# Kernel optimization log

Hardware: AMD Instinct MI355X
Metric: run time of the kernel (lower is better)

Reference implementation:

```python
import jax, jax.numpy as jnp
import numpy as np

NUM_HEADS = 8

def _proj(x, w, b):
    # 1x1x1 Conv3d == pointwise linear over channel dim
    return jnp.einsum('bcxyz,oc->boxyz', x, w) + b[None, :, None, None, None]


def setup_inputs() -> dict:
    key = jax.random.key(0)
    ks = jax.random.split(key, 9)
    B, C, X, Y, Z = 2, 256, 48, 48, 48
    s = 0.05
    return {
        'x':  jax.random.normal(ks[0], (B, C, X, Y, Z), dtype=jnp.float32),
        'wq': jax.random.normal(ks[1], (C, C), dtype=jnp.float32) * s,
        'bq': jax.random.normal(ks[2], (C,), dtype=jnp.float32) * s,
        'wk': jax.random.normal(ks[3], (C, C), dtype=jnp.float32) * s,
        'bk': jax.random.normal(ks[4], (C,), dtype=jnp.float32) * s,
        'wv': jax.random.normal(ks[5], (C, C), dtype=jnp.float32) * s,
        'bv': jax.random.normal(ks[6], (C,), dtype=jnp.float32) * s,
        'wo': jax.random.normal(ks[7], (C, C), dtype=jnp.float32) * s,
        'bo': jax.random.normal(ks[8], (C,), dtype=jnp.float32) * s,
    }


def reference(x, wq, bq, wk, bk, wv, bv, wo, bo):
    B, C, X, Y, Z = x.shape
    H = NUM_HEADS
    P = C // H  # per-head channels
    q = _proj(x, wq, bq).reshape(B, H, P, X, Y, Z)
    k = _proj(x, wk, bk).reshape(B, H, P, X, Y, Z)
    v = _proj(x, wv, bv).reshape(B, H, P, X, Y, Z)
    # torch einsum 'bnxyzc,bmxyzc->bnmxy' contracts z and per-head channel c
    scores = jnp.einsum('bncxyz,bmcxyz->bnmxy', q, k) / jnp.sqrt(jnp.float32(P))
    # torch F.softmax(dim=-1) on [b,n,m,x,y] -> softmax over y axis (faithful)
    attn = jax.nn.softmax(scores, axis=-1)
    # torch 'bnmxy,bmxyzc->bnxyzc', then permute/reshape back to [B,C,X,Y,Z]
    out = jnp.einsum('bnmxy,bmcxyz->bncxyz', attn, v).reshape(B, C, X, Y, Z)
    return _proj(out, wo, bo)
```

## Files before the change

kernel.cpp:

```cpp
#include <hip/hip_runtime.h>
#include <hip/hip_bf16.h>
#include <stdint.h>


#define S_TOT 110592
#define NBX   2304

typedef unsigned short u16;
typedef __attribute__((ext_vector_type(8))) short bf16x8;
typedef __attribute__((ext_vector_type(4))) float f32x4;

__device__ __forceinline__ u16 f2b(float f){
  union { float f; uint32_t u; } v; v.f = f;
  uint32_t u = v.u;
  return (u16)((u + 0x7fffu + ((u >> 16) & 1u)) >> 16);
}
__device__ __forceinline__ float b2f(u16 h){
  union { float f; uint32_t u; } v; v.u = ((uint32_t)h) << 16; return v.f;
}
__device__ __forceinline__ f32x4 mfma16(bf16x8 a, bf16x8 b, f32x4 c){
  return __builtin_amdgcn_mfma_f32_16x16x32_bf16(a, b, c, 0, 0, 0);
}

__global__ __launch_bounds__(256) void k_prep(
    const float* __restrict__ wq, const float* __restrict__ wk,
    const float* __restrict__ wv, const float* __restrict__ wo,
    u16* __restrict__ img)
{
  int idx = blockIdx.x * 256 + threadIdx.x;
  if (idx < 131072){
    int ck = idx >> 14, rem = idx & 16383;
    int r = rem >> 5, i = rem & 31;
    int c = ck * 32 + i;
    float v = (r < 256) ? wq[r * 256 + c] : wk[(r - 256) * 256 + c];
    img[idx] = f2b(v);
  } else if (idx < 196608){
    int l = idx - 131072;
    int ck = l >> 13, rem = l & 8191;
    int r = rem >> 5, i = rem & 31;
    img[idx] = f2b(wv[r * 256 + ck * 32 + i]);
  } else if (idx < 262144){
    int l = idx - 196608;
    int ck = l >> 13, rem = l & 8191;
    int r = rem >> 5, i = rem & 31;
    img[idx] = f2b(wo[r * 256 + ck * 32 + i]);
  }
}

#define K1_LDS 57344
__global__ __launch_bounds__(1024, 4) void k_qk_scores(
    const float* __restrict__ x, const u16* __restrict__ wimg,
    const float* __restrict__ bq, const float* __restrict__ bk,
    float* __restrict__ scores)
{
  extern __shared__ char lds[];
  u16* xT  = (u16*)lds;
  u16* qkz = (u16*)lds;
  float* ps0 = (float*)(lds + 49152);
  float* ps1 = (float*)(lds + 53248);

  const int tid  = threadIdx.x;
  const int wave = tid >> 6, lane = tid & 63;
  const int l15 = lane & 15, l4 = lane >> 4;
  const int bx = blockIdx.x, b = blockIdx.y;
  const int s0 = bx * 96;
  const float* xb = x + (size_t)b * 256 * S_TOT;

  #pragma unroll
  for (int it = 0; it < 3; it++){
    int e = it * 1024 + tid;
    int z = e % 96, c16 = e / 96;
    const float* px = xb + (size_t)(c16 * 8) * S_TOT + s0 + z;
    union { uint4 q; u16 h[8]; } u;
    #pragma unroll
    for (int i = 0; i < 8; i++) u.h[i] = f2b(px[(size_t)i * S_TOT]);
    *(uint4*)((char*)xT + z * 512 + ((c16 ^ (z & 7)) << 4)) = u.q;
  }
  __syncthreads();

  const int proj = wave >> 3;
  const int rb = (wave & 7) * 32;
  const float* bias = proj ? bk : bq;

  f32x4 acc[2][6];
  #pragma unroll
  for (int fr = 0; fr < 2; fr++){
    f32x4 iv;
    #pragma unroll
    for (int j = 0; j < 4; j++) iv[j] = bias[rb + fr * 16 + l4 * 4 + j];
    #pragma unroll
    for (int fc = 0; fc < 6; fc++) acc[fr][fc] = iv;
  }
  #pragma unroll
  for (int ck = 0; ck < 8; ck++){
    bf16x8 af[2], bfr[6];
    #pragma unroll
    for (int fr = 0; fr < 2; fr++){
      int row = wave * 32 + fr * 16 + l15;
      af[fr] = *(const bf16x8*)(wimg + ck * 16384 + row * 32 + l4 * 8);
    }
    #pragma unroll
    for (int fc = 0; fc < 6; fc++){
      int z = fc * 16 + l15;
      bfr[fc] = *(const bf16x8*)((char*)xT + z * 512 + (((ck * 4 + l4) ^ (l15 & 7)) << 4));
    }
    #pragma unroll
    for (int fr = 0; fr < 2; fr++)
      #pragma unroll
      for (int fc = 0; fc < 6; fc++)
        acc[fr][fc] = mfma16(af[fr], bfr[fc], acc[fr][fc]);
  }
  __syncthreads();

  const int och = proj * 256 + rb + l4 * 4;
  const int ca = l15 * 32 + l4 * 8;
  const int cb = 256 + (l15 & 7) * 32 + l4 * 8;

  #pragma unroll
  for (int fr = 0; fr < 2; fr++){
    int oc = och + fr * 16;
    #pragma unroll
    for (int fc = 0; fc < 3; fc++){
      int zl = fc * 16 + l15;
      ushort4 u;
      u.x = f2b(acc[fr][fc][0]); u.y = f2b(acc[fr][fc][1]);
      u.z = f2b(acc[fr][fc][2]); u.w = f2b(acc[fr][fc][3]);
      *(ushort4*)((char*)qkz + zl * 1024 + ((((oc >> 3) ^ zl) & 63) << 4)
                  + (oc & 7) * 2) = u;
    }
  }
  __syncthreads();
  {
    f32x4 sc = {0.f, 0.f, 0.f, 0.f};
    #pragma unroll
    for (int zi = 0; zi < 3; zi++){
      int zl = wave * 3 + zi;
      bf16x8 aq  = *(const bf16x8*)((char*)qkz + zl * 1024 + ((((ca >> 3) ^ zl) & 63) << 4));
      bf16x8 bk8 = *(const bf16x8*)((char*)qkz + zl * 1024 + ((((cb >> 3) ^ zl) & 63) << 4));
      sc = mfma16(aq, bk8, sc);
    }
    if (l4 < 2 && l15 < 8){
      #pragma unroll
      for (int j = 0; j < 4; j++)
        ps0[wave * 64 + (l4 * 4 + j) * 8 + l15] = sc[j];
    }
  }
  __syncthreads();

  if (tid < 64){
    float s = 0.f;
    #pragma unroll
    for (int w = 0; w < 16; w++) s += ps0[w * 64 + tid];
    scores[(size_t)(b * 64 + tid) * NBX + bx * 2] = s * 0.17677669529663687f;
  }
  #pragma unroll
  for (int fr = 0; fr < 2; fr++){
    int oc = och + fr * 16;
    #pragma unroll
    for (int fc = 3; fc < 6; fc++){
      int zl = (fc - 3) * 16 + l15;
      ushort4 u;
      u.x = f2b(acc[fr][fc][0]); u.y = f2b(acc[fr][fc][1]);
      u.z = f2b(acc[fr][fc][2]); u.w = f2b(acc[fr][fc][3]);
      *(ushort4*)((char*)qkz + zl * 1024 + ((((oc >> 3) ^ zl) & 63) << 4)
                  + (oc & 7) * 2) = u;
    }
  }
  __syncthreads();
  {
    f32x4 sc = {0.f, 0.f, 0.f, 0.f};
    #pragma unroll
    for (int zi = 0; zi < 3; zi++){
      int zl = wave * 3 + zi;
      bf16x8 aq  = *(const bf16x8*)((char*)qkz + zl * 1024 + ((((ca >> 3) ^ zl) & 63) << 4));
      bf16x8 bk8 = *(const bf16x8*)((char*)qkz + zl * 1024 + ((((cb >> 3) ^ zl) & 63) << 4));
      sc = mfma16(aq, bk8, sc);
    }
    if (l4 < 2 && l15 < 8){
      #pragma unroll
      for (int j = 0; j < 4; j++)
        ps1[wave * 64 + (l4 * 4 + j) * 8 + l15] = sc[j];
    }
  }
  __syncthreads();
  if (tid < 64){
    float s = 0.f;
    #pragma unroll
    for (int w = 0; w < 16; w++) s += ps1[w * 64 + tid];
    scores[(size_t)(b * 64 + tid) * NBX + bx * 2 + 1] = s * 0.17677669529663687f;
  }
}

__global__ __launch_bounds__(256) void k_softmax(
    const float* __restrict__ scores, float* __restrict__ attn)
{
  int row  = blockIdx.x * 4 + (threadIdx.x >> 6);
  int lane = threadIdx.x & 63;
  const float* src = scores + (size_t)row * 48;
  float v = (lane < 48) ? src[lane] : -1e30f;
  float m = v;
  #pragma unroll
  for (int off = 32; off; off >>= 1) m = fmaxf(m, __shfl_xor(m, off));
  float e = (lane < 48) ? __expf(v - m) : 0.f;
  float s = e;
  #pragma unroll
  for (int off = 32; off; off >>= 1) s += __shfl_xor(s, off);
  if (lane < 48) attn[(size_t)row * 48 + lane] = e / s;
}

#define K3_LDS 49664
__global__ __launch_bounds__(512, 4) void k_out(
    const float* __restrict__ x, const u16* __restrict__ wvimg,
    const u16* __restrict__ woimg, const float* __restrict__ bv,
    const float* __restrict__ bo, const float* __restrict__ attn,
    float* __restrict__ out)
{
  extern __shared__ char lds[];
  u16* xT = (u16*)lds;
  u16* vl = (u16*)lds;
  u16* oT = (u16*)lds;
  float* atl = (float*)(lds + 49152);

  const int tid  = threadIdx.x;
  const int wave = tid >> 6, lane = tid & 63;
  const int l15 = lane & 15, l4 = lane >> 4;
  const int bx = blockIdx.x, b = blockIdx.y;
  const int s0 = bx * 96;
  const float* xb = x + (size_t)b * 256 * S_TOT;

  if (tid < 128)
    atl[tid] = attn[(size_t)(b * 64 + (tid & 63)) * NBX + bx * 2 + (tid >> 6)];

  #pragma unroll
  for (int it = 0; it < 6; it++){
    int e = it * 512 + tid;
    int z = e % 96, c16 = e / 96;
    const float* px = xb + (size_t)(c16 * 8) * S_TOT + s0 + z;
    union { uint4 q; u16 h[8]; } u;
    #pragma unroll
    for (int i = 0; i < 8; i++) u.h[i] = f2b(px[(size_t)i * S_TOT]);
    *(uint4*)((char*)xT + z * 512 + ((c16 ^ (z & 7)) << 4)) = u.q;
  }
  __syncthreads();

  f32x4 vac[2][6];
  #pragma unroll
  for (int fr = 0; fr < 2; fr++){
    f32x4 iv;
    #pragma unroll
    for (int j = 0; j < 4; j++) iv[j] = bv[wave * 32 + fr * 16 + l4 * 4 + j];
    #pragma unroll
    for (int fc = 0; fc < 6; fc++) vac[fr][fc] = iv;
  }
  #pragma unroll
  for (int ck = 0; ck < 8; ck++){
    bf16x8 af[2], bfr[6];
    #pragma unroll
    for (int fr = 0; fr < 2; fr++){
      int row = wave * 32 + fr * 16 + l15;
      af[fr] = *(const bf16x8*)(wvimg + ck * 8192 + row * 32 + l4 * 8);
    }
    #pragma unroll
    for (int fc = 0; fc < 6; fc++){
      int z = fc * 16 + l15;
      bfr[fc] = *(const bf16x8*)((char*)xT + z * 512 + (((ck * 4 + l4) ^ (l15 & 7)) << 4));
    }
    #pragma unroll
    for (int fr = 0; fr < 2; fr++)
      #pragma unroll
      for (int fc = 0; fc < 6; fc++)
        vac[fr][fc] = mfma16(af[fr], bfr[fc], vac[fr][fc]);
  }
  __syncthreads();

  #pragma unroll
  for (int fr = 0; fr < 2; fr++){
    int o0 = wave * 32 + fr * 16 + l4 * 4;
    #pragma unroll
    for (int fc = 0; fc < 6; fc++){
      int z = fc * 16 + l15;
      ushort4 u;
      u.x = f2b(vac[fr][fc][0]); u.y = f2b(vac[fr][fc][1]);
      u.z = f2b(vac[fr][fc][2]); u.w = f2b(vac[fr][fc][3]);
      *(ushort4*)((char*)vl + z * 512 + (((o0 >> 3) ^ (z & 7)) << 4) + (o0 & 7) * 2) = u;
    }
  }
  __syncthreads();

  #pragma unroll
  for (int it = 0; it < 6; it++){
    int e = it * 512 + tid;
    int c16 = e & 31, z = e >> 5;
    int r = c16 & 3, hn = c16 >> 2;
    const float* at = atl + ((z >= 48) ? 64 : 0);
    float a[8] = {0,0,0,0,0,0,0,0};
    #pragma unroll
    for (int m = 0; m < 8; m++){
      union { uint4 q; u16 h[8]; } v8;
      v8.q = *(const uint4*)((char*)vl + z * 512 + (((m * 4 + r) ^ (z & 7)) << 4));
      float am = at[hn * 8 + m];
      #pragma unroll
      for (int i = 0; i < 8; i++) a[i] = fmaf(am, b2f(v8.h[i]), a[i]);
    }
    union { uint4 q; u16 h[8]; } pk;
    #pragma unroll
    for (int i = 0; i < 8; i++) pk.h[i] = f2b(a[i]);
    __syncthreads();
    *(uint4*)((char*)oT + z * 512 + ((c16 ^ (z & 7)) << 4)) = pk.q;
  }
  __syncthreads();

  f32x4 oac[2][6];
  #pragma unroll
  for (int fr = 0; fr < 2; fr++){
    f32x4 iv;
    #pragma unroll
    for (int j = 0; j < 4; j++) iv[j] = bo[wave * 32 + fr * 16 + l4 * 4 + j];
    #pragma unroll
    for (int fc = 0; fc < 6; fc++) oac[fr][fc] = iv;
  }
  #pragma unroll
  for (int ck = 0; ck < 8; ck++){
    bf16x8 af[2], bfr[6];
    #pragma unroll
    for (int fr = 0; fr < 2; fr++){
      int row = wave * 32 + fr * 16 + l15;
      af[fr] = *(const bf16x8*)(woimg + ck * 8192 + row * 32 + l4 * 8);
    }
    #pragma unroll
    for (int fc = 0; fc < 6; fc++){
      int z = fc * 16 + l15;
      bfr[fc] = *(const bf16x8*)((char*)oT + z * 512 + (((ck * 4 + l4) ^ (l15 & 7)) << 4));
    }
    #pragma unroll
    for (int fr = 0; fr < 2; fr++)
      #pragma unroll
      for (int fc = 0; fc < 6; fc++)
        oac[fr][fc] = mfma16(af[fr], bfr[fc], oac[fr][fc]);
  }

  #pragma unroll
  for (int fr = 0; fr < 2; fr++)
    #pragma unroll
    for (int fc = 0; fc < 6; fc++)
      #pragma unroll
      for (int j = 0; j < 4; j++){
        int o = wave * 32 + fr * 16 + l4 * 4 + j;
        int z = fc * 16 + l15;
        __builtin_nontemporal_store(oac[fr][fc][j],
            &out[(size_t)(b * 256 + o) * S_TOT + s0 + z]);
      }
}

extern "C" void kernel_launch(void* const* d_in, const int* in_sizes, int n_in,
                              void* d_out, int out_size, void* d_ws, size_t ws_size,
                              hipStream_t stream) {
  (void)in_sizes; (void)n_in; (void)out_size; (void)ws_size;
  const float* x  = (const float*)d_in[0];
  const float* wq = (const float*)d_in[1];
  const float* bq = (const float*)d_in[2];
  const float* wk = (const float*)d_in[3];
  const float* bk = (const float*)d_in[4];
  const float* wv = (const float*)d_in[5];
  const float* bv = (const float*)d_in[6];
  const float* wo = (const float*)d_in[7];
  const float* bo = (const float*)d_in[8];
  float* out = (float*)d_out;

  char* ws = (char*)d_ws;
  u16*  wimg   = (u16*)ws;
  u16*  wvimg  = wimg + 131072;
  u16*  woimg  = wimg + 196608;
  float* scores = (float*)(ws + 524288);
  float* attn   = (float*)(ws + 1703936);

  k_prep<<<1024, 256, 0, stream>>>(wq, wk, wv, wo, wimg);
  k_qk_scores<<<dim3(1152, 2), 1024, K1_LDS, stream>>>(x, wimg, bq, bk, scores);
  k_softmax<<<1536, 256, 0, stream>>>(scores, attn);
  k_out<<<dim3(1152, 2), 512, K3_LDS, stream>>>(x, wvimg, woimg, bv, bo, attn, out);
}
```

Measured before the change: 221.0 us.

## Compute V projection in first pass and stash bf16 V in workspace

Adds a fused kernel that converts x to bf16 once and computes Q, K scores and the V projection in the same block, writing V as bf16 tiles to the workspace. The output kernel then reads the precomputed bf16 V instead of re-reading fp32 x and redoing the V GEMM. The goal is to cut the second full fp32 read of x and the duplicated conversion. In exchange it writes and reads back about 113 MB of V, and the first kernel uses 148 KB of LDS, which limits occupancy to one block per CU. The path is only taken when the workspace is large enough.

```diff
diff --git a/kernel.cpp b/kernel.cpp
--- a/kernel.cpp
+++ b/kernel.cpp
@@ -47,6 +47,151 @@
   }
 }
 
+#define K1F_LDS 151552
+__global__ __launch_bounds__(1024, 4) void k_qkv(
+    const float* __restrict__ x, const u16* __restrict__ wimg,
+    const u16* __restrict__ wvimg,
+    const float* __restrict__ bq, const float* __restrict__ bk,
+    const float* __restrict__ bv,
+    float* __restrict__ scores, u16* __restrict__ vws)
+{
+  extern __shared__ char lds[];
+  u16* xT  = (u16*)lds;
+  u16* qkz = (u16*)(lds + 49152);
+  float* ps = (float*)(lds + 147456);
+
+  const int tid  = threadIdx.x;
+  const int wave = tid >> 6, lane = tid & 63;
+  const int l15 = lane & 15, l4 = lane >> 4;
+  const int bx = blockIdx.x, b = blockIdx.y;
+  const int s0 = bx * 96;
+  const float* xb = x + (size_t)b * 256 * S_TOT;
+
+  #pragma unroll
+  for (int it = 0; it < 3; it++){
+    int e = it * 1024 + tid;
+    int z = e % 96, c16 = e / 96;
+    const float* px = xb + (size_t)(c16 * 8) * S_TOT + s0 + z;
+    union { uint4 q; u16 h[8]; } u;
+    #pragma unroll
+    for (int i = 0; i < 8; i++) u.h[i] = f2b(px[(size_t)i * S_TOT]);
+    *(uint4*)((char*)xT + z * 512 + ((c16 ^ (z & 7)) << 4)) = u.q;
+  }
+  __syncthreads();
+
+  const int proj = wave >> 3;
+  const int rb = (wave & 7) * 32;
+  const float* bias = proj ? bk : bq;
+
+  f32x4 acc[2][6];
+  #pragma unroll
+  for (int fr = 0; fr < 2; fr++){
+    f32x4 iv;
+    #pragma unroll
+    for (int j = 0; j < 4; j++) iv[j] = bias[rb + fr * 16 + l4 * 4 + j];
+    #pragma unroll
+    for (int fc = 0; fc < 6; fc++) acc[fr][fc] = iv;
+  }
+  #pragma unroll
+  for (int ck = 0; ck < 8; ck++){
+    bf16x8 af[2], bfr[6];
+    #pragma unroll
+    for (int fr = 0; fr < 2; fr++){
+      int row = wave * 32 + fr * 16 + l15;
+      af[fr] = *(const bf16x8*)(wimg + ck * 16384 + row * 32 + l4 * 8);
+    }
+    #pragma unroll
+    for (int fc = 0; fc < 6; fc++){
+      int z = fc * 16 + l15;
+      bfr[fc] = *(const bf16x8*)((char*)xT + z * 512 + (((ck * 4 + l4) ^ (l15 & 7)) << 4));
+    }
+    #pragma unroll
+    for (int fr = 0; fr < 2; fr++)
+      #pragma unroll
+      for (int fc = 0; fc < 6; fc++)
+        acc[fr][fc] = mfma16(af[fr], bfr[fc], acc[fr][fc]);
+  }
+
+  #pragma unroll
+  for (int fr = 0; fr < 2; fr++){
+    int och = proj * 256 + rb + fr * 16 + l4 * 4;
+    #pragma unroll
+    for (int fc = 0; fc < 6; fc++){
+      int z = fc * 16 + l15;
+      ushort4 u;
+      u.x = f2b(acc[fr][fc][0]); u.y = f2b(acc[fr][fc][1]);
+      u.z = f2b(acc[fr][fc][2]); u.w = f2b(acc[fr][fc][3]);
+      *(ushort4*)((char*)qkz + z * 1024 + ((((och >> 3) ^ z) & 63) << 4)
+                  + (och & 7) * 2) = u;
+    }
+  }
+  __syncthreads();
+
+  {
+    const int ca = l15 * 32 + l4 * 8;
+    const int cb = 256 + (l15 & 7) * 32 + l4 * 8;
+    const int zb = (wave >> 3) * 48 + (wave & 7) * 6;
+    f32x4 sc = {0.f, 0.f, 0.f, 0.f};
+    #pragma unroll
+    for (int zi = 0; zi < 6; zi++){
+      int zl = zb + zi;
+      bf16x8 aq  = *(const bf16x8*)((char*)qkz + zl * 1024 + ((((ca >> 3) ^ zl) & 63) << 4));
+      bf16x8 bk8 = *(const bf16x8*)((char*)qkz + zl * 1024 + ((((cb >> 3) ^ zl) & 63) << 4));
+      sc = mfma16(aq, bk8, sc);
+    }
+    if (l4 < 2 && l15 < 8){
+      #pragma unroll
+      for (int j = 0; j < 4; j++)
+        ps[wave * 64 + (l4 * 4 + j) * 8 + l15] = sc[j];
+    }
+  }
+  __syncthreads();
+
+  if (tid < 128){
+    int h = tid >> 6, idx = tid & 63;
+    float s = 0.f;
+    #pragma unroll
+    for (int w = 0; w < 8; w++) s += ps[(h * 8 + w) * 64 + idx];
+    scores[(size_t)(b * 64 + idx) * NBX + bx * 2 + h] = s * 0.17677669529663687f;
+  }
+
+  f32x4 vac[6];
+  {
+    f32x4 iv;
+    #pragma unroll
+    for (int j = 0; j < 4; j++) iv[j] = bv[wave * 16 + l4 * 4 + j];
+    #pragma unroll
+    for (int fc = 0; fc < 6; fc++) vac[fc] = iv;
+  }
+  #pragma unroll
+  for (int ck = 0; ck < 8; ck++){
+    bf16x8 af, bfr[6];
+    af = *(const bf16x8*)(wvimg + ck * 8192 + (wave * 16 + l15) * 32 + l4 * 8);
+    #pragma unroll
+    for (int fc = 0; fc < 6; fc++){
+      int z = fc * 16 + l15;
+      bfr[fc] = *(const bf16x8*)((char*)xT + z * 512 + (((ck * 4 + l4) ^ (l15 & 7)) << 4));
+    }
+    #pragma unroll
+    for (int fc = 0; fc < 6; fc++)
+      vac[fc] = mfma16(af, bfr[fc], vac[fc]);
+  }
+
+  {
+    u16* vt = vws + (size_t)(b * 1152 + bx) * 24576;
+    int ch0 = wave * 16 + l4 * 4;
+    #pragma unroll
+    for (int fc = 0; fc < 6; fc++){
+      int z = fc * 16 + l15;
+      ushort4 u;
+      u.x = f2b(vac[fc][0]); u.y = f2b(vac[fc][1]);
+      u.z = f2b(vac[fc][2]); u.w = f2b(vac[fc][3]);
+      *(ushort4*)((char*)vt + z * 512 + ((((ch0 >> 3) ^ (z & 7)) & 31) << 4)
+                  + (ch0 & 7) * 2) = u;
+    }
+  }
+}
+
 #define K1_LDS 57344
 __global__ __launch_bounds__(1024, 4) void k_qk_scores(
     const float* __restrict__ x, const u16* __restrict__ wimg,
@@ -146,7 +291,6 @@
     }
   }
   __syncthreads();
-
   if (tid < 64){
     float s = 0.f;
     #pragma unroll
@@ -209,6 +353,98 @@
 }
 
 #define K3_LDS 49664
+__global__ __launch_bounds__(512, 4) void k_out_v(
+    const u16* __restrict__ vws, const u16* __restrict__ woimg,
+    const float* __restrict__ bo, const float* __restrict__ attn,
+    float* __restrict__ out)
+{
+  extern __shared__ char lds[];
+  u16* vl = (u16*)lds;
+  u16* oT = (u16*)lds;
+  float* atl = (float*)(lds + 49152);
+
+  const int tid  = threadIdx.x;
+  const int wave = tid >> 6, lane = tid & 63;
+  const int l15 = lane & 15, l4 = lane >> 4;
+  const int bx = blockIdx.x, b = blockIdx.y;
+  const int s0 = bx * 96;
+
+  if (tid < 128)
+    atl[tid] = attn[(size_t)(b * 64 + (tid & 63)) * NBX + bx * 2 + (tid >> 6)];
+
+  {
+    const uint4* vt = (const uint4*)(vws + (size_t)(b * 1152 + bx) * 24576);
+    #pragma unroll
+    for (int it = 0; it < 6; it++)
+      ((uint4*)vl)[it * 512 + tid] = vt[it * 512 + tid];
+  }
+  __syncthreads();
+
+  #pragma unroll
+  for (int it = 0; it < 6; it++){
+    int e = it * 512 + tid;
+    int c16 = e & 31, z = e >> 5;
+    int r = c16 & 3, hn = c16 >> 2;
+    const float* at = atl + ((z >= 48) ? 64 : 0);
+    float a[8] = {0,0,0,0,0,0,0,0};
+    #pragma unroll
+    for (int m = 0; m < 8; m++){
+      union { uint4 q; u16 h[8]; } v8;
+      v8.q = *(const uint4*)((char*)vl + z * 512 + (((m * 4 + r) ^ (z & 7)) << 4));
+      float am = at[hn * 8 + m];
+      #pragma unroll
+      for (int i = 0; i < 8; i++) a[i] = fmaf(am, b2f(v8.h[i]), a[i]);
+    }
+    union { uint4 q; u16 h[8]; } pk;
+    #pragma unroll
+    for (int i = 0; i < 8; i++) pk.h[i] = f2b(a[i]);
+    __syncthreads();
+    *(uint4*)((char*)oT + z * 512 + ((c16 ^ (z & 7)) << 4)) = pk.q;
+  }
+  __syncthreads();
+
+  f32x4 oac[2][6];
+  #pragma unroll
+  for (int fr = 0; fr < 2; fr++){
+    f32x4 iv;
+    #pragma unroll
+    for (int j = 0; j < 4; j++) iv[j] = bo[wave * 32 + fr * 16 + l4 * 4 + j];
+    #pragma unroll
+    for (int fc = 0; fc < 6; fc++) oac[fr][fc] = iv;
+  }
+  #pragma unroll
+  for (int ck = 0; ck < 8; ck++){
+    bf16x8 af[2], bfr[6];
+    #pragma unroll
+    for (int fr = 0; fr < 2; fr++){
+      int row = wave * 32 + fr * 16 + l15;
+      af[fr] = *(const bf16x8*)(woimg + ck * 8192 + row * 32 + l4 * 8);
+    }
+    #pragma unroll
+    for (int fc = 0; fc < 6; fc++){
+      int z = fc * 16 + l15;
+      bfr[fc] = *(const bf16x8*)((char*)oT + z * 512 + (((ck * 4 + l4) ^ (l15 & 7)) << 4));
+    }
+    #pragma unroll
+    for (int fr = 0; fr < 2; fr++)
+      #pragma unroll
+      for (int fc = 0; fc < 6; fc++)
+        oac[fr][fc] = mfma16(af[fr], bfr[fc], oac[fr][fc]);
+  }
+
+  #pragma unroll
+  for (int fr = 0; fr < 2; fr++)
+    #pragma unroll
+    for (int fc = 0; fc < 6; fc++)
+      #pragma unroll
+      for (int j = 0; j < 4; j++){
+        int o = wave * 32 + fr * 16 + l4 * 4 + j;
+        int z = fc * 16 + l15;
+        __builtin_nontemporal_store(oac[fr][fc][j],
+            &out[(size_t)(b * 256 + o) * S_TOT + s0 + z]);
+      }
+}
+
 __global__ __launch_bounds__(512, 4) void k_out(
     const float* __restrict__ x, const u16* __restrict__ wvimg,
     const u16* __restrict__ woimg, const float* __restrict__ bv,
@@ -355,7 +591,7 @@
 extern "C" void kernel_launch(void* const* d_in, const int* in_sizes, int n_in,
                               void* d_out, int out_size, void* d_ws, size_t ws_size,
                               hipStream_t stream) {
-  (void)in_sizes; (void)n_in; (void)out_size; (void)ws_size;
+  (void)in_sizes; (void)n_in; (void)out_size;
   const float* x  = (const float*)d_in[0];
   const float* wq = (const float*)d_in[1];
   const float* bq = (const float*)d_in[2];
@@ -373,9 +609,25 @@
   u16*  woimg  = wimg + 196608;
   float* scores = (float*)(ws + 524288);
   float* attn   = (float*)(ws + 1703936);
+  u16*  vws     = (u16*)(ws + 2883584);
+
+  const size_t need = 2883584 + 113246208;
+  const bool fused = (ws_size >= need);
 
   k_prep<<<1024, 256, 0, stream>>>(wq, wk, wv, wo, wimg);
-  k_qk_scores<<<dim3(1152, 2), 1024, K1_LDS, stream>>>(x, wimg, bq, bk, scores);
+  if (fused){
+    hipFuncSetAttribute((const void*)k_qkv,
+                        hipFuncAttributeMaxDynamicSharedMemorySize, K1F_LDS);
+    k_qkv<<<dim3(1152, 2), 1024, K1F_LDS, stream>>>(
+        x, wimg, wvimg, bq, bk, bv, scores, vws);
+  } else {
+    k_qk_scores<<<dim3(1152, 2), 1024, K1_LDS, stream>>>(x, wimg, bq, bk, scores);
+  }
   k_softmax<<<1536, 256, 0, stream>>>(scores, attn);
-  k_out<<<dim3(1152, 2), 512, K3_LDS, stream>>>(x, wvimg, woimg, bv, bo, attn, out);
-}
+  if (fused){
+    k_out_v<<<dim3(1152, 2), 512, K3_LDS, stream>>>(vws, woimg, bo, attn, out);
+  } else {
+    k_out<<<dim3(1152, 2), 512, K3_LDS, stream>>>(
+        x, wvimg, woimg, bv, bo, attn, out);
+  }
+}
```

Result: slower. 231.2 us (+4.6%).
